# Kernel tuning notes

Measured on AMD Instinct MI355X. Metric: run time of the kernel, lower is better.

Reference implementation:

```python
import jax, jax.numpy as jnp
import numpy as np

N = 100000   # nodes
E = 1600000  # edges
NC = 10000   # candidates
G = 1000     # graphs
ND = 32      # node_emb_dim
ED = 8       # edge_emb_dim
L = 4        # num_layers


def setup_inputs() -> dict:
    key = jax.random.key(0)
    ks = jax.random.split(key, 12)
    s = 0.1
    return {
        "x": jax.random.normal(ks[0], (N, 2), dtype=jnp.float32),
        "edge_attr": jax.random.normal(ks[1], (E, 1), dtype=jnp.float32),
        "Wn_in": jax.random.normal(ks[2], (2, ND)) * s,
        "bn_in": jnp.zeros((ND,)),
        "We_in": jax.random.normal(ks[3], (1, ED)) * s,
        "be_in": jnp.zeros((ED,)),
        "We_l": jax.random.normal(ks[4], (L, 2 * ND + ED, ED)) * s,
        "be_l": jnp.zeros((L, ED)),
        "Wn_l": jax.random.normal(ks[5], (L, ND + ED, ND)) * s,
        "bn_l": jnp.zeros((L, ND)),
        "Wout": jax.random.normal(ks[6], (ND, 1)) * s,
        "bout": jnp.zeros((1,)),
        "edge_index": jax.random.randint(ks[7], (2, E), 0, N),
        "batch": jnp.sort(jax.random.randint(ks[8], (N,), 0, G)),
        "candidate_idxs": jax.random.randint(ks[9], (NC,), 0, N),
    }


def reference(x, edge_attr, Wn_in, bn_in, We_in, be_in, We_l, be_l, Wn_l, bn_l,
              Wout, bout, edge_index, batch, candidate_idxs):
    h = x @ Wn_in + bn_in            # [N, ND]
    e = edge_attr @ We_in + be_in    # [E, ED]
    src, dst = edge_index[0], edge_index[1]
    for l in range(L):
        # edge update: MLP on [x_src, x_dst, edge_attr]
        m = jnp.concatenate([h[src], h[dst], e], axis=-1)        # [E, 2*ND+ED]
        new_e = jax.nn.relu(m @ We_l[l] + be_l[l])               # [E, ED]
        # aggregate (aggr='add') messages at destination nodes
        agg = jax.ops.segment_sum(new_e, dst, num_segments=N)    # [N, ED]
        new_h = jax.nn.relu(jnp.concatenate([h, agg], axis=-1) @ Wn_l[l] + bn_l[l])
        h = h + new_h   # residual
        e = e + new_e   # residual
    logits = (h[candidate_idxs] @ Wout + bout)[:, 0]             # [NC]
    seg = batch[candidate_idxs]                                  # [NC] graph ids
    # scatter_log_softmax over per-graph candidate groups
    mx = jax.ops.segment_max(logits, seg, num_segments=G)
    shifted = logits - mx[seg]
    lse = jnp.log(jax.ops.segment_sum(jnp.exp(shifted), seg, num_segments=G))
    return shifted - lse[seg]
```

## Files before the change

### kernel.cpp

```cpp
#include <hip/hip_runtime.h>

#define ND 32
#define ED 8
#define NL 4
#define NG 1000
#define NBC_MAX 512
#define CHUNK 8192
#define CHUNK_H 4096
#define NBLK 64

typedef unsigned short u16;

__device__ __forceinline__ int xcd_swizzle(int b, int nb) {
  int per = nb >> 3;
  return (b < (per << 3)) ? ((b & 7) * per + (b >> 3)) : b;
}


__device__ __forceinline__ unsigned pack2(float a, float b) {
  unsigned r;
  asm("v_cvt_pk_bf16_f32 %0, %1, %2" : "=v"(r) : "v"(a), "v"(b));
  return r;
}
__device__ __forceinline__ float bf_round(float f) {
  unsigned r;
  asm("v_cvt_pk_bf16_f32 %0, %1, %2" : "=v"(r) : "v"(f), "v"(f));
  return __uint_as_float(r << 16);
}
__device__ __forceinline__ void cvt8(uint4 p, float* o) {
  o[0] = __uint_as_float(p.x << 16); o[1] = __uint_as_float(p.x & 0xffff0000u);
  o[2] = __uint_as_float(p.y << 16); o[3] = __uint_as_float(p.y & 0xffff0000u);
  o[4] = __uint_as_float(p.z << 16); o[5] = __uint_as_float(p.z & 0xffff0000u);
  o[6] = __uint_as_float(p.w << 16); o[7] = __uint_as_float(p.w & 0xffff0000u);
}
__device__ __forceinline__ uint4 pack8(const float* v) {
  uint4 o;
  o.x = pack2(v[0], v[1]); o.y = pack2(v[2], v[3]);
  o.z = pack2(v[4], v[5]); o.w = pack2(v[6], v[7]);
  return o;
}


__global__ void k_init_h(const float* __restrict__ x,
                         const float* __restrict__ W,
                         const float* __restrict__ b,
                         const float* __restrict__ We,
                         const float* __restrict__ be,
                         u16* __restrict__ h,
                         u16* __restrict__ zs, u16* __restrict__ zd,
                         int N) {
  int n = xcd_swizzle(blockIdx.x, gridDim.x) * blockDim.x + threadIdx.x;
  if (n >= N) return;
  float x0 = x[2 * n], x1 = x[2 * n + 1];
  float v[ND];
#pragma unroll
  for (int d = 0; d < ND; ++d) v[d] = fmaf(x0, W[d], fmaf(x1, W[ND + d], b[d]));
#pragma unroll
  for (int d = 0; d < ND; ++d) v[d] = bf_round(v[d]);
  uint4* h4 = reinterpret_cast<uint4*>(h + (size_t)n * ND);
#pragma unroll
  for (int q = 0; q < 4; ++q) h4[q] = pack8(&v[q * 8]);
  float zsv[ED], zdv[ED];
#pragma unroll
  for (int j = 0; j < ED; ++j) { zsv[j] = 0.0f; zdv[j] = be[j]; }
#pragma unroll
  for (int k = 0; k < ND; ++k)
#pragma unroll
    for (int j = 0; j < ED; ++j) {
      zsv[j] = fmaf(v[k], We[k * ED + j], zsv[j]);
      zdv[j] = fmaf(v[k], We[(ND + k) * ED + j], zdv[j]);
    }
  *reinterpret_cast<uint4*>(zs + (size_t)n * ED) = pack8(zsv);
  *reinterpret_cast<uint4*>(zd + (size_t)n * ED) = pack8(zdv);
}


__global__ void k_chist(const int* __restrict__ dst, int* __restrict__ bcnt,
                        int E, int nbc) {
  __shared__ int lcnt[NBC_MAX];
  for (int b = threadIdx.x; b < nbc; b += blockDim.x) lcnt[b] = 0;
  __syncthreads();
  int e0 = blockIdx.x * CHUNK_H;
  int e1 = min(e0 + CHUNK_H, E);
  for (int i = e0 + threadIdx.x; i < e1; i += blockDim.x)
    atomicAdd(&lcnt[dst[i] >> 8], 1);
  __syncthreads();
  for (int b = threadIdx.x; b < nbc; b += blockDim.x)
    if (lcnt[b]) atomicAdd(&bcnt[b], lcnt[b]);
}

__global__ void k_cscan(const int* __restrict__ bcnt, int* __restrict__ bbase,
                        int nbc) {
  __shared__ int s[NBC_MAX];
  int tid = threadIdx.x;
  if (nbc <= NBC_MAX) {
    int v = (tid < nbc) ? bcnt[tid] : 0;
    s[tid] = v;
    __syncthreads();
    for (int st = 1; st < NBC_MAX; st <<= 1) {
      int t = (tid >= st) ? s[tid - st] : 0;
      __syncthreads();
      s[tid] += t;
      __syncthreads();
    }
    if (tid < nbc) bbase[tid] = s[tid] - v;
    if (tid == nbc - 1) bbase[nbc] = s[tid];
  } else if (tid == 0) {
    int run = 0;
    for (int i = 0; i < nbc; ++i) { bbase[i] = run; run += bcnt[i]; }
    bbase[nbc] = run;
  }
}

__global__ void k_binA(const int* __restrict__ src, const int* __restrict__ dst,
                       const float* __restrict__ ea,
                       const int* __restrict__ bbase, int* __restrict__ cursor_c,
                       uint2* __restrict__ binned, int E, int nbc) {
  __shared__ int lcnt[NBC_MAX];
  __shared__ int lbase[NBC_MAX];
  for (int b = threadIdx.x; b < nbc; b += blockDim.x) lcnt[b] = 0;
  __syncthreads();
  int e0 = blockIdx.x * CHUNK;
  int e1 = min(e0 + CHUNK, E);
  for (int i = e0 + threadIdx.x; i < e1; i += blockDim.x)
    atomicAdd(&lcnt[dst[i] >> 8], 1);
  __syncthreads();
  for (int b = threadIdx.x; b < nbc; b += blockDim.x) {
    int c = lcnt[b];
    lbase[b] = c ? (bbase[b] + atomicAdd(&cursor_c[b], c)) : 0;
  }
  __syncthreads();
  for (int i = e0 + threadIdx.x; i < e1; i += blockDim.x) {
    int d = dst[i];
    int pos = atomicAdd(&lbase[d >> 8], 1);
    binned[pos] = make_uint2((unsigned)src[i] | ((unsigned)(d & 255) << 24),
                             __float_as_uint(ea[i]));
  }
}

__global__ void k_binB(const uint2* __restrict__ binned,
                       const int* __restrict__ bbase,
                       int* __restrict__ ssrc, float* __restrict__ ea_s,
                       int* __restrict__ noffs,
                       int N) {
  __shared__ int hist[256];
  __shared__ int scn[256];
  int b = blockIdx.x;
  int base = bbase[b], end = bbase[b + 1];
  int node0 = b << 8;
  int nn = min(256, N - node0);
  hist[threadIdx.x] = 0;
  __syncthreads();
  for (int p = base + threadIdx.x; p < end; p += blockDim.x)
    atomicAdd(&hist[binned[p].x >> 24], 1);
  __syncthreads();
  int v = hist[threadIdx.x];
  scn[threadIdx.x] = v;
  __syncthreads();
  for (int st = 1; st < 256; st <<= 1) {
    int t = (threadIdx.x >= (unsigned)st) ? scn[threadIdx.x - st] : 0;
    __syncthreads();
    scn[threadIdx.x] += t;
    __syncthreads();
  }
  int excl = base + scn[threadIdx.x] - v;
  if ((int)threadIdx.x < nn) noffs[node0 + threadIdx.x] = excl;
  if (threadIdx.x == 0) noffs[min(node0 + 256, N)] = end;
  hist[threadIdx.x] = excl;
  __syncthreads();
  for (int p = base + threadIdx.x; p < end; p += blockDim.x) {
    uint2 rec = binned[p];
    int dl = (int)(rec.x >> 24);
    int pos = atomicAdd(&hist[dl], 1);
    ssrc[pos] = (int)(rec.x & 0xffffffu);
    ea_s[pos] = __uint_as_float(rec.y);
  }
}

template <int L0>
__global__ void k_layer(u16* __restrict__ h,
                        u16* __restrict__ e,
                        const float* __restrict__ ea_s,
                        const int* __restrict__ ssrc,
                        const int* __restrict__ noffs,
                        const u16* __restrict__ zs,
                        const u16* __restrict__ zd,
                        const float* __restrict__ Wei,
                        const float* __restrict__ bei,
                        const float* __restrict__ W3,
                        const float* __restrict__ Wn,
                        const float* __restrict__ bn,
                        const float* __restrict__ Wen,
                        const float* __restrict__ ben,
                        u16* __restrict__ zs_n, u16* __restrict__ zd_n,
                        int N) {
  int t = xcd_swizzle(blockIdx.x, gridDim.x) * blockDim.x + threadIdx.x;
  int n = t >> 3;
  int g = t & 7;
  if (n >= N) return;
  int o0 = noffs[n], o1 = noffs[n + 1];
  uint4* h4 = reinterpret_cast<uint4*>(h + (size_t)n * ND);
  uint4 hq0 = h4[0], hq1 = h4[1], hq2 = h4[2], hq3 = h4[3];
  float zdv[ED];
  cvt8(*reinterpret_cast<const uint4*>(zd + (size_t)n * ED), zdv);
  const uint4* zs4 = reinterpret_cast<const uint4*>(zs);
  const uint4* e4c = reinterpret_cast<const uint4*>(e);
  uint4* e4 = reinterpret_cast<uint4*>(e);
  float av[ED];
#pragma unroll
  for (int j = 0; j < ED; ++j) av[j] = 0.0f;

  auto edge_one = [&](int p_, uint4 z_, uint4 e_, float a_) {
    float zsv[ED], ein[ED], acc[ED];
    cvt8(z_, zsv);
    if (L0) {
#pragma unroll
      for (int j = 0; j < ED; ++j) ein[j] = fmaf(a_, Wei[j], bei[j]);
    } else {
      cvt8(e_, ein);
    }
#pragma unroll
    for (int j = 0; j < ED; ++j) acc[j] = zsv[j] + zdv[j];
#pragma unroll
    for (int k = 0; k < ED; ++k)
#pragma unroll
      for (int j = 0; j < ED; ++j)
        acc[j] = fmaf(ein[k], W3[k * ED + j], acc[j]);
    float eo[ED];
#pragma unroll
    for (int j = 0; j < ED; ++j) {
      float r = fmaxf(acc[j], 0.0f);
      av[j] += r;
      eo[j] = ein[j] + r;
    }
    e4[p_] = pack8(eo);
  };

  for (int base = o0 + g; base < o1; base += 32) {
    bool v1 = base + 8 < o1, v2 = base + 16 < o1, v3 = base + 24 < o1;
    int pa = base;
    int pb = v1 ? base + 8 : base;
    int pc = v2 ? base + 16 : base;
    int pd = v3 ? base + 24 : base;
    int sa = ssrc[pa], sb = ssrc[pb], sc = ssrc[pc], sd = ssrc[pd];
    uint4 Ea = make_uint4(0, 0, 0, 0), Eb = Ea, Ec = Ea, Ed = Ea;
    float Aa = 0.f, Ab = 0.f, Ac = 0.f, Ad = 0.f;
    if (L0) {
      Aa = ea_s[pa]; Ab = ea_s[pb]; Ac = ea_s[pc]; Ad = ea_s[pd];
    } else {
      Ea = e4c[pa]; Eb = e4c[pb]; Ec = e4c[pc]; Ed = e4c[pd];
    }
    uint4 Za = zs4[sa], Zb = zs4[sb], Zc = zs4[sc], Zd = zs4[sd];
    edge_one(pa, Za, Ea, Aa);
    if (v1) edge_one(pb, Zb, Eb, Ab);
    if (v2) edge_one(pc, Zc, Ec, Ac);
    if (v3) edge_one(pd, Zd, Ed, Ad);
  }
#pragma unroll
  for (int j = 0; j < ED; ++j) {
    av[j] += __shfl_xor(av[j], 1);
    av[j] += __shfl_xor(av[j], 2);
    av[j] += __shfl_xor(av[j], 4);
  }
  float hv[ND];
  cvt8(hq0, &hv[0]); cvt8(hq1, &hv[8]); cvt8(hq2, &hv[16]); cvt8(hq3, &hv[24]);
  const int j0 = g * 4;
  float acc4[4];
#pragma unroll
  for (int jj = 0; jj < 4; ++jj) acc4[jj] = bn[j0 + jj];
#pragma unroll
  for (int k = 0; k < ND; ++k)
#pragma unroll
    for (int jj = 0; jj < 4; ++jj)
      acc4[jj] = fmaf(hv[k], Wn[k * ND + j0 + jj], acc4[jj]);
#pragma unroll
  for (int k = 0; k < ED; ++k)
#pragma unroll
    for (int jj = 0; jj < 4; ++jj)
      acc4[jj] = fmaf(av[k], Wn[(ND + k) * ND + j0 + jj], acc4[jj]);
  float hn4[4];
#pragma unroll
  for (int jj = 0; jj < 4; ++jj)
    hn4[jj] = bf_round(hv[j0 + jj] + fmaxf(acc4[jj], 0.0f));
  reinterpret_cast<uint2*>(h + (size_t)n * ND)[g] =
      make_uint2(pack2(hn4[0], hn4[1]), pack2(hn4[2], hn4[3]));
  float pz[2 * ED];
#pragma unroll
  for (int j = 0; j < 2 * ED; ++j) pz[j] = 0.0f;
#pragma unroll
  for (int kk = 0; kk < 4; ++kk) {
    float hk = hn4[kk];
    int krow = j0 + kk;
#pragma unroll
    for (int j = 0; j < ED; ++j) {
      pz[j] = fmaf(hk, Wen[krow * ED + j], pz[j]);
      pz[ED + j] = fmaf(hk, Wen[(ND + krow) * ED + j], pz[ED + j]);
    }
  }
#pragma unroll
  for (int j = 0; j < 2 * ED; ++j) {
    pz[j] += __shfl_xor(pz[j], 1);
    pz[j] += __shfl_xor(pz[j], 2);
    pz[j] += __shfl_xor(pz[j], 4);
  }
  if (g == 0) {
    *reinterpret_cast<uint4*>(zs_n + (size_t)n * ED) = pack8(pz);
  } else if (g == 1) {
    float zdo[ED];
#pragma unroll
    for (int j = 0; j < ED; ++j) zdo[j] = pz[ED + j] + ben[j];
    *reinterpret_cast<uint4*>(zd_n + (size_t)n * ED) = pack8(zdo);
  }
}


__device__ __forceinline__ unsigned int enc_f32(float f) {
  unsigned int bits = __float_as_uint(f);
  return (bits & 0x80000000u) ? ~bits : (bits | 0x80000000u);
}
__device__ __forceinline__ float dec_f32(unsigned int u) {
  unsigned int bits = (u & 0x80000000u) ? (u ^ 0x80000000u) : ~u;
  return __uint_as_float(bits);
}

__global__ void k_cand(const u16* __restrict__ h,
                       const u16* __restrict__ e,
                       const u16* __restrict__ zs,
                       const u16* __restrict__ zd,
                       const int* __restrict__ ssrc,
                       const int* __restrict__ noffs,
                       const int* __restrict__ cand,
                       const int* __restrict__ batch,
                       const float* __restrict__ W3,
                       const float* __restrict__ Wn,
                       const float* __restrict__ bn,
                       const float* __restrict__ Wout,
                       const float* __restrict__ bout,
                       float* __restrict__ logits,
                       int* __restrict__ seg,
                       unsigned int* __restrict__ mxu,
                       int NC) {
  int t = blockIdx.x * blockDim.x + threadIdx.x;
  int c = t >> 4, g = t & 15;
  if (c >= NC) return;
  int n = cand[c];
  int o0 = noffs[n], o1 = noffs[n + 1];
  const uint4* h4 = reinterpret_cast<const uint4*>(h + (size_t)n * ND);
  uint4 hq0 = h4[0], hq1 = h4[1], hq2 = h4[2], hq3 = h4[3];
  float zdv[ED];
  cvt8(*reinterpret_cast<const uint4*>(zd + (size_t)n * ED), zdv);
  const uint4* zs4 = reinterpret_cast<const uint4*>(zs);
  const uint4* e4c = reinterpret_cast<const uint4*>(e);
  float av[ED];
#pragma unroll
  for (int j = 0; j < ED; ++j) av[j] = 0.0f;

  auto cand_one = [&](uint4 z_, uint4 e_) {
    float zsv[ED], ein[ED], acc[ED];
    cvt8(z_, zsv);
    cvt8(e_, ein);
#pragma unroll
    for (int j = 0; j < ED; ++j) acc[j] = zsv[j] + zdv[j];
#pragma unroll
    for (int k = 0; k < ED; ++k)
#pragma unroll
      for (int j = 0; j < ED; ++j)
        acc[j] = fmaf(ein[k], W3[k * ED + j], acc[j]);
#pragma unroll
    for (int j = 0; j < ED; ++j) av[j] += fmaxf(acc[j], 0.0f);
  };

  for (int base = o0 + g; base < o1; base += 32) {
    bool v1 = base + 16 < o1;
    int pa = base;
    int pb = v1 ? base + 16 : base;
    int sa = ssrc[pa], sb = ssrc[pb];
    uint4 Ea = e4c[pa], Eb = e4c[pb];
    uint4 Za = zs4[sa], Zb = zs4[sb];
    cand_one(Za, Ea);
    if (v1) cand_one(Zb, Eb);
  }
#pragma unroll
  for (int j = 0; j < ED; ++j) {
    av[j] += __shfl_xor(av[j], 1);
    av[j] += __shfl_xor(av[j], 2);
    av[j] += __shfl_xor(av[j], 4);
    av[j] += __shfl_xor(av[j], 8);
  }
  float hv[ND];
  cvt8(hq0, &hv[0]); cvt8(hq1, &hv[8]); cvt8(hq2, &hv[16]); cvt8(hq3, &hv[24]);
  const int j0 = g * 2;
  float acc2[2];
#pragma unroll
  for (int jj = 0; jj < 2; ++jj) acc2[jj] = bn[j0 + jj];
#pragma unroll
  for (int k = 0; k < ND; ++k)
#pragma unroll
    for (int jj = 0; jj < 2; ++jj)
      acc2[jj] = fmaf(hv[k], Wn[k * ND + j0 + jj], acc2[jj]);
#pragma unroll
  for (int k = 0; k < ED; ++k)
#pragma unroll
    for (int jj = 0; jj < 2; ++jj)
      acc2[jj] = fmaf(av[k], Wn[(ND + k) * ND + j0 + jj], acc2[jj]);
  float lg = 0.0f;
#pragma unroll
  for (int jj = 0; jj < 2; ++jj)
    lg = fmaf(hv[j0 + jj] + fmaxf(acc2[jj], 0.0f), Wout[j0 + jj], lg);
  lg += __shfl_xor(lg, 1);
  lg += __shfl_xor(lg, 2);
  lg += __shfl_xor(lg, 4);
  lg += __shfl_xor(lg, 8);
  if (g == 0) {
    lg += bout[0];
    logits[c] = lg;
    int gr = batch[n];
    seg[c] = gr;
    atomicMax(&mxu[gr], enc_f32(lg));
  }
}

__global__ void k_expsum(float* __restrict__ logits,
                         const int* __restrict__ seg,
                         const unsigned int* __restrict__ mxu,
                         float* __restrict__ sum,
                         int NC) {
  int c = blockIdx.x * blockDim.x + threadIdx.x;
  if (c >= NC) return;
  int g = seg[c];
  float sh = logits[c] - dec_f32(mxu[g]);
  logits[c] = sh;
  atomicAdd(&sum[g], expf(sh));
}

__global__ void k_final(const float* __restrict__ shifted,
                        const int* __restrict__ seg,
                        const float* __restrict__ sum,
                        float* __restrict__ out, int NC) {
  int c = blockIdx.x * blockDim.x + threadIdx.x;
  if (c >= NC) return;
  out[c] = shifted[c] - logf(sum[seg[c]]);
}


extern "C" void kernel_launch(void* const* d_in, const int* in_sizes, int n_in,
                              void* d_out, int out_size, void* d_ws, size_t ws_size,
                              hipStream_t stream) {
  const float* x       = (const float*)d_in[0];
  const float* ea      = (const float*)d_in[1];
  const float* Wn_in   = (const float*)d_in[2];
  const float* bn_in   = (const float*)d_in[3];
  const float* We_in   = (const float*)d_in[4];
  const float* be_in   = (const float*)d_in[5];
  const float* We_l    = (const float*)d_in[6];
  const float* be_l    = (const float*)d_in[7];
  const float* Wn_l    = (const float*)d_in[8];
  const float* bn_l    = (const float*)d_in[9];
  const float* Wout    = (const float*)d_in[10];
  const float* bout    = (const float*)d_in[11];
  const int* edge_index= (const int*)d_in[12];
  const int* batch     = (const int*)d_in[13];
  const int* cand      = (const int*)d_in[14];

  const int N  = in_sizes[13];
  const int E  = in_sizes[1];
  const int NC = in_sizes[14];
  const int nbc = (N + 255) >> 8;

  char* ws = (char*)d_ws;
  uint2* binned = (uint2*)ws; ws += (size_t)E * sizeof(uint2);
  int*   ssrc   = (int*)ws;   ws += (size_t)E * sizeof(int);
  float* ea_s   = (float*)ws; ws += (size_t)E * sizeof(float);
  u16*   h      = (u16*)ws;   ws += (size_t)N * ND * sizeof(u16);
  u16*   e      = (u16*)ws;   ws += (size_t)E * ED * sizeof(u16);
  u16*   zs0    = (u16*)ws;   ws += (size_t)N * ED * sizeof(u16);
  u16*   zd0    = (u16*)ws;   ws += (size_t)N * ED * sizeof(u16);
  u16*   zs1    = (u16*)ws;   ws += (size_t)N * ED * sizeof(u16);
  u16*   zd1    = (u16*)ws;   ws += (size_t)N * ED * sizeof(u16);
  int*   noffs  = (int*)ws;   ws += ((size_t)N + 4) * sizeof(int);
  int*   bcnt   = (int*)ws;   ws += (size_t)NBC_MAX * sizeof(int);
  int*   cursor = (int*)ws;   ws += (size_t)NBC_MAX * sizeof(int);
  int*   bbase  = (int*)ws;   ws += ((size_t)NBC_MAX + 4) * sizeof(int);
  float* logits = (float*)ws; ws += (size_t)NC * sizeof(float);
  int*   seg    = (int*)ws;   ws += (size_t)NC * sizeof(int);
  unsigned int* mxu = (unsigned int*)ws; ws += (size_t)NG * sizeof(unsigned int);
  float* sum    = (float*)ws; ws += (size_t)NG * sizeof(float);

  const int* srcp = edge_index;
  const int* dstp = edge_index + E;
  const int blk = 256;
  const size_t WE_STRIDE = (size_t)(2 * ND + ED) * ED;

  hipMemsetAsync(bcnt, 0, 2 * (size_t)NBC_MAX * sizeof(int), stream);
  k_chist<<<(E + CHUNK_H - 1) / CHUNK_H, 1024, 0, stream>>>(dstp, bcnt, E, nbc);
  k_cscan<<<1, NBC_MAX, 0, stream>>>(bcnt, bbase, nbc);
  k_binA<<<(E + CHUNK - 1) / CHUNK, 1024, 0, stream>>>(srcp, dstp, ea, bbase,
                                                       cursor, binned, E, nbc);
  k_binB<<<nbc, 256, 0, stream>>>(binned, bbase, ssrc, ea_s, noffs, N);

  k_init_h<<<(N + NBLK - 1) / NBLK, NBLK, 0, stream>>>(x, Wn_in, bn_in, We_l,
                                                       be_l, h, zs0, zd0, N);

  const int ngrid8 = (N + 31) / 32;
  u16* zsc = zs0; u16* zdc = zd0;
  u16* zsn = zs1; u16* zdn = zd1;
  for (int l = 0; l < NL - 1; ++l) {
    const float* W3 = We_l + l * WE_STRIDE + (size_t)2 * ND * ED;
    const float* Wn = Wn_l + (size_t)l * (ND + ED) * ND;
    const float* bn = bn_l + (size_t)l * ND;
    const float* Wen = We_l + (l + 1) * WE_STRIDE;
    const float* ben = be_l + (size_t)(l + 1) * ED;
    if (l == 0) {
      k_layer<1><<<ngrid8, 256, 0, stream>>>(
          h, e, ea_s, ssrc, noffs, zsc, zdc, We_in, be_in, W3, Wn, bn,
          Wen, ben, zsn, zdn, N);
    } else {
      k_layer<0><<<ngrid8, 256, 0, stream>>>(
          h, e, ea_s, ssrc, noffs, zsc, zdc, We_in, be_in, W3, Wn, bn,
          Wen, ben, zsn, zdn, N);
    }
    u16* t;
    t = zsc; zsc = zsn; zsn = t;
    t = zdc; zdc = zdn; zdn = t;
  }

  hipMemsetAsync(mxu, 0, NG * (sizeof(unsigned int) + sizeof(float)), stream);
  {
    const int l = NL - 1;
    const float* W3 = We_l + l * WE_STRIDE + (size_t)2 * ND * ED;
    const float* Wn = Wn_l + (size_t)l * (ND + ED) * ND;
    const float* bn = bn_l + (size_t)l * ND;
    k_cand<<<((size_t)NC * 16 + 255) / 256, 256, 0, stream>>>(
        h, e, zsc, zdc, ssrc, noffs, cand, batch, W3, Wn, bn, Wout, bout,
        logits, seg, mxu, NC);
  }
  k_expsum<<<(NC + blk - 1) / blk, blk, 0, stream>>>(logits, seg, mxu, sum, NC);
  k_final<<<(NC + blk - 1) / blk, blk, 0, stream>>>(logits, seg, sum,
                                                    (float*)d_out, NC);
}
```

Baseline: 347.6 us.

## Fuse node init into binning, software-pipeline edge loop, merge memsets

```diff
diff --git a/kernel.cpp b/kernel.cpp
--- a/kernel.cpp
+++ b/kernel.cpp
@@ -7,7 +7,6 @@
 #define NBC_MAX 512
 #define CHUNK 8192
 #define CHUNK_H 4096
-#define NBLK 64
 
 typedef unsigned short u16;
 
@@ -38,40 +37,6 @@
   o.x = pack2(v[0], v[1]); o.y = pack2(v[2], v[3]);
   o.z = pack2(v[4], v[5]); o.w = pack2(v[6], v[7]);
   return o;
-}
-
-
-__global__ void k_init_h(const float* __restrict__ x,
-                         const float* __restrict__ W,
-                         const float* __restrict__ b,
-                         const float* __restrict__ We,
-                         const float* __restrict__ be,
-                         u16* __restrict__ h,
-                         u16* __restrict__ zs, u16* __restrict__ zd,
-                         int N) {
-  int n = xcd_swizzle(blockIdx.x, gridDim.x) * blockDim.x + threadIdx.x;
-  if (n >= N) return;
-  float x0 = x[2 * n], x1 = x[2 * n + 1];
-  float v[ND];
-#pragma unroll
-  for (int d = 0; d < ND; ++d) v[d] = fmaf(x0, W[d], fmaf(x1, W[ND + d], b[d]));
-#pragma unroll
-  for (int d = 0; d < ND; ++d) v[d] = bf_round(v[d]);
-  uint4* h4 = reinterpret_cast<uint4*>(h + (size_t)n * ND);
-#pragma unroll
-  for (int q = 0; q < 4; ++q) h4[q] = pack8(&v[q * 8]);
-  float zsv[ED], zdv[ED];
-#pragma unroll
-  for (int j = 0; j < ED; ++j) { zsv[j] = 0.0f; zdv[j] = be[j]; }
-#pragma unroll
-  for (int k = 0; k < ND; ++k)
-#pragma unroll
-    for (int j = 0; j < ED; ++j) {
-      zsv[j] = fmaf(v[k], We[k * ED + j], zsv[j]);
-      zdv[j] = fmaf(v[k], We[(ND + k) * ED + j], zdv[j]);
-    }
-  *reinterpret_cast<uint4*>(zs + (size_t)n * ED) = pack8(zsv);
-  *reinterpret_cast<uint4*>(zd + (size_t)n * ED) = pack8(zdv);
 }
 
 
@@ -138,11 +103,18 @@
   }
 }
 
-__global__ void k_binB(const uint2* __restrict__ binned,
-                       const int* __restrict__ bbase,
-                       int* __restrict__ ssrc, float* __restrict__ ea_s,
-                       int* __restrict__ noffs,
-                       int N) {
+__global__ void k_binB_init(const uint2* __restrict__ binned,
+                            const int* __restrict__ bbase,
+                            int* __restrict__ ssrc, float* __restrict__ ea_s,
+                            int* __restrict__ noffs,
+                            const float* __restrict__ x,
+                            const float* __restrict__ Wni,
+                            const float* __restrict__ bni,
+                            const float* __restrict__ We0,
+                            const float* __restrict__ be0,
+                            u16* __restrict__ h,
+                            u16* __restrict__ zs, u16* __restrict__ zd,
+                            int N) {
   __shared__ int hist[256];
   __shared__ int scn[256];
   int b = blockIdx.x;
@@ -174,6 +146,29 @@
     int pos = atomicAdd(&hist[dl], 1);
     ssrc[pos] = (int)(rec.x & 0xffffffu);
     ea_s[pos] = __uint_as_float(rec.y);
+  }
+  int n = node0 + threadIdx.x;
+  if (n < N) {
+    float x0 = x[2 * n], x1 = x[2 * n + 1];
+    float vv[ND];
+#pragma unroll
+    for (int d = 0; d < ND; ++d)
+      vv[d] = bf_round(fmaf(x0, Wni[d], fmaf(x1, Wni[ND + d], bni[d])));
+    uint4* h4 = reinterpret_cast<uint4*>(h + (size_t)n * ND);
+#pragma unroll
+    for (int q = 0; q < 4; ++q) h4[q] = pack8(&vv[q * 8]);
+    float zsv[ED], zdv[ED];
+#pragma unroll
+    for (int j = 0; j < ED; ++j) { zsv[j] = 0.0f; zdv[j] = be0[j]; }
+#pragma unroll
+    for (int k = 0; k < ND; ++k)
+#pragma unroll
+      for (int j = 0; j < ED; ++j) {
+        zsv[j] = fmaf(vv[k], We0[k * ED + j], zsv[j]);
+        zdv[j] = fmaf(vv[k], We0[(ND + k) * ED + j], zdv[j]);
+      }
+    *reinterpret_cast<uint4*>(zs + (size_t)n * ED) = pack8(zsv);
+    *reinterpret_cast<uint4*>(zd + (size_t)n * ED) = pack8(zdv);
   }
 }
 
@@ -199,8 +194,6 @@
   int g = t & 7;
   if (n >= N) return;
   int o0 = noffs[n], o1 = noffs[n + 1];
-  uint4* h4 = reinterpret_cast<uint4*>(h + (size_t)n * ND);
-  uint4 hq0 = h4[0], hq1 = h4[1], hq2 = h4[2], hq3 = h4[3];
   float zdv[ED];
   cvt8(*reinterpret_cast<const uint4*>(zd + (size_t)n * ED), zdv);
   const uint4* zs4 = reinterpret_cast<const uint4*>(zs);
@@ -210,14 +203,36 @@
 #pragma unroll
   for (int j = 0; j < ED; ++j) av[j] = 0.0f;
 
-  auto edge_one = [&](int p_, uint4 z_, uint4 e_, float a_) {
+  int p = o0 + g;
+  int sA = 0, sB = 0;
+  uint4 eA = make_uint4(0, 0, 0, 0), eB = make_uint4(0, 0, 0, 0);
+  float aA = 0.0f, aB = 0.0f;
+  uint4 zA = make_uint4(0, 0, 0, 0);
+  if (p < o1) {
+    sA = ssrc[p];
+    if (L0) aA = ea_s[p]; else eA = e4c[p];
+    zA = zs4[sA];
+  }
+  if (p + 8 < o1) {
+    sB = ssrc[p + 8];
+    if (L0) aB = ea_s[p + 8]; else eB = e4c[p + 8];
+  }
+  for (; p < o1; ) {
+    int pn = p + 8, pc = p + 16;
+    uint4 zB = make_uint4(0, 0, 0, 0);
+    if (pn < o1) zB = zs4[sB];
+    int sC = 0; uint4 eC = make_uint4(0, 0, 0, 0); float aC = 0.0f;
+    if (pc < o1) {
+      sC = ssrc[pc];
+      if (L0) aC = ea_s[pc]; else eC = e4c[pc];
+    }
     float zsv[ED], ein[ED], acc[ED];
-    cvt8(z_, zsv);
+    cvt8(zA, zsv);
     if (L0) {
 #pragma unroll
-      for (int j = 0; j < ED; ++j) ein[j] = fmaf(a_, Wei[j], bei[j]);
+      for (int j = 0; j < ED; ++j) ein[j] = fmaf(aA, Wei[j], bei[j]);
     } else {
-      cvt8(e_, ein);
+      cvt8(eA, ein);
     }
 #pragma unroll
     for (int j = 0; j < ED; ++j) acc[j] = zsv[j] + zdv[j];
@@ -233,28 +248,10 @@
       av[j] += r;
       eo[j] = ein[j] + r;
     }
-    e4[p_] = pack8(eo);
-  };
-
-  for (int base = o0 + g; base < o1; base += 32) {
-    bool v1 = base + 8 < o1, v2 = base + 16 < o1, v3 = base + 24 < o1;
-    int pa = base;
-    int pb = v1 ? base + 8 : base;
-    int pc = v2 ? base + 16 : base;
-    int pd = v3 ? base + 24 : base;
-    int sa = ssrc[pa], sb = ssrc[pb], sc = ssrc[pc], sd = ssrc[pd];
-    uint4 Ea = make_uint4(0, 0, 0, 0), Eb = Ea, Ec = Ea, Ed = Ea;
-    float Aa = 0.f, Ab = 0.f, Ac = 0.f, Ad = 0.f;
-    if (L0) {
-      Aa = ea_s[pa]; Ab = ea_s[pb]; Ac = ea_s[pc]; Ad = ea_s[pd];
-    } else {
-      Ea = e4c[pa]; Eb = e4c[pb]; Ec = e4c[pc]; Ed = e4c[pd];
-    }
-    uint4 Za = zs4[sa], Zb = zs4[sb], Zc = zs4[sc], Zd = zs4[sd];
-    edge_one(pa, Za, Ea, Aa);
-    if (v1) edge_one(pb, Zb, Eb, Ab);
-    if (v2) edge_one(pc, Zc, Ec, Ac);
-    if (v3) edge_one(pd, Zd, Ed, Ad);
+    e4[p] = pack8(eo);
+    p = pn;
+    sA = sB; eA = eB; aA = aB; zA = zB;
+    sB = sC; eB = eC; aB = aC;
   }
 #pragma unroll
   for (int j = 0; j < ED; ++j) {
@@ -262,8 +259,10 @@
     av[j] += __shfl_xor(av[j], 2);
     av[j] += __shfl_xor(av[j], 4);
   }
+  uint4* h4 = reinterpret_cast<uint4*>(h + (size_t)n * ND);
   float hv[ND];
-  cvt8(hq0, &hv[0]); cvt8(hq1, &hv[8]); cvt8(hq2, &hv[16]); cvt8(hq3, &hv[24]);
+#pragma unroll
+  for (int q = 0; q < 4; ++q) cvt8(h4[q], &hv[q * 8]);
   const int j0 = g * 4;
   float acc4[4];
 #pragma unroll
@@ -480,26 +479,27 @@
   int*   noffs  = (int*)ws;   ws += ((size_t)N + 4) * sizeof(int);
   int*   bcnt   = (int*)ws;   ws += (size_t)NBC_MAX * sizeof(int);
   int*   cursor = (int*)ws;   ws += (size_t)NBC_MAX * sizeof(int);
+  unsigned int* mxu = (unsigned int*)ws; ws += (size_t)NG * sizeof(unsigned int);
+  float* sum    = (float*)ws; ws += (size_t)NG * sizeof(float);
   int*   bbase  = (int*)ws;   ws += ((size_t)NBC_MAX + 4) * sizeof(int);
   float* logits = (float*)ws; ws += (size_t)NC * sizeof(float);
   int*   seg    = (int*)ws;   ws += (size_t)NC * sizeof(int);
-  unsigned int* mxu = (unsigned int*)ws; ws += (size_t)NG * sizeof(unsigned int);
-  float* sum    = (float*)ws; ws += (size_t)NG * sizeof(float);
 
   const int* srcp = edge_index;
   const int* dstp = edge_index + E;
   const int blk = 256;
   const size_t WE_STRIDE = (size_t)(2 * ND + ED) * ED;
 
-  hipMemsetAsync(bcnt, 0, 2 * (size_t)NBC_MAX * sizeof(int), stream);
+  hipMemsetAsync(bcnt, 0, (2 * (size_t)NBC_MAX + 2 * (size_t)NG) * sizeof(int),
+                 stream);
+
   k_chist<<<(E + CHUNK_H - 1) / CHUNK_H, 1024, 0, stream>>>(dstp, bcnt, E, nbc);
   k_cscan<<<1, NBC_MAX, 0, stream>>>(bcnt, bbase, nbc);
   k_binA<<<(E + CHUNK - 1) / CHUNK, 1024, 0, stream>>>(srcp, dstp, ea, bbase,
                                                        cursor, binned, E, nbc);
-  k_binB<<<nbc, 256, 0, stream>>>(binned, bbase, ssrc, ea_s, noffs, N);
-
-  k_init_h<<<(N + NBLK - 1) / NBLK, NBLK, 0, stream>>>(x, Wn_in, bn_in, We_l,
-                                                       be_l, h, zs0, zd0, N);
+  k_binB_init<<<nbc, 256, 0, stream>>>(binned, bbase, ssrc, ea_s, noffs,
+                                       x, Wn_in, bn_in, We_l, be_l,
+                                       h, zs0, zd0, N);
 
   const int ngrid8 = (N + 31) / 32;
   u16* zsc = zs0; u16* zdc = zd0;
@@ -524,7 +524,6 @@
     t = zdc; zdc = zdn; zdn = t;
   }
 
-  hipMemsetAsync(mxu, 0, NG * (sizeof(unsigned int) + sizeof(float)), stream);
   {
     const int l = NL - 1;
     const float* W3 = We_l + l * WE_STRIDE + (size_t)2 * ND * ED;
```

After: 331.8 us (median of 3 runs). 4.5% less time.
